# Kernel tuning notes

Hardware: AMD Instinct MI355X
Metric: run time of the kernel (lower is better)

## Reference

```python
import jax, jax.numpy as jnp
import numpy as np

TEMPERATURE = 0.6


def setup_inputs() -> dict:
    key = jax.random.key(0)
    k1, k2, k3 = jax.random.split(key, 3)
    B, IN, OUT, C = 8192, 256, 32, 50
    x = jax.random.uniform(k1, (B, IN), dtype=jnp.float32)
    weight = jax.random.normal(k2, (C, OUT, IN), dtype=jnp.float32) * 0.05
    bias = jax.random.normal(k3, (C, 1, OUT), dtype=jnp.float32) * 0.05
    return {"x": x, "weight": weight, "bias": bias}


def reference(x, weight, bias):
    # gamma[c,i] = L1 norm of weight over out dim: sum_o |W[c,o,i]|
    gamma = jnp.sum(jnp.abs(weight), axis=1)            # [C, IN]
    alpha = jax.nn.softmax(gamma / TEMPERATURE, axis=1)  # [C, IN]
    alpha_norm = alpha / jnp.max(alpha, axis=1, keepdims=True)  # [C, IN]
    # gated input per class: [C, B, IN]
    xg = x[None, :, :] * alpha_norm[:, None, :]
    # per-class GEMM: y[c,b,o] = sum_i xg[c,b,i] * W[c,o,i]
    y = jnp.einsum('cbi,coi->cbo', xg, weight) + bias    # [C, B, OUT]
    return jnp.transpose(y, (1, 0, 2))                   # [B, C, OUT]
```

## Files before the change

kernel.cpp:

```cpp
#include <hip/hip_runtime.h>
#include <hip/hip_bf16.h>

typedef __bf16 bf16x8 __attribute__((ext_vector_type(8)));
typedef float  f32x4  __attribute__((ext_vector_type(4)));

#define B_ROWS 8192
#define IN_DIM 256
#define OUT_DIM 32
#define NCLS 50
#define INV_T (1.0f / 0.6f)

#define CVT_BLOCKS 1024
#define PG_BLOCKS 400
#define ROWTILES 16
#define NCHUNK 8

__device__ __forceinline__ void gload_lds16(const void* g, void* l) {
    __builtin_amdgcn_global_load_lds(
        (const __attribute__((address_space(1))) void*)g,
        (__attribute__((address_space(3))) void*)l, 16, 0, 0);
}

__global__ __launch_bounds__(256) void k1_cvt_partial(const float* __restrict__ x,
                                                      const float* __restrict__ w,
                                                      __bf16* __restrict__ xb,
                                                      float* __restrict__ partial) {
    int bid = blockIdx.x;
    if (bid < CVT_BLOCKS) {
        int i = (bid * 256 + threadIdx.x) * 8;
        float4 v0 = *reinterpret_cast<const float4*>(x + i);
        float4 v1 = *reinterpret_cast<const float4*>(x + i + 4);
        bf16x8 r;
        r[0] = (__bf16)v0.x; r[1] = (__bf16)v0.y; r[2] = (__bf16)v0.z; r[3] = (__bf16)v0.w;
        r[4] = (__bf16)v1.x; r[5] = (__bf16)v1.y; r[6] = (__bf16)v1.z; r[7] = (__bf16)v1.w;
        *reinterpret_cast<bf16x8*>(xb + i) = r;
    } else {
        int p = bid - CVT_BLOCKS;
        int c = p >> 3, q = p & 7;
        int i = threadIdx.x;
        const float* wp = w + ((size_t)(c * OUT_DIM + q * 4)) * IN_DIM + i;
        float g = fabsf(wp[0]) + fabsf(wp[IN_DIM]) + fabsf(wp[2 * IN_DIM]) + fabsf(wp[3 * IN_DIM]);
        partial[(size_t)p * IN_DIM + i] = g;
    }
}

__global__ __launch_bounds__(256) void k2_alpha_scale(const float* __restrict__ partial,
                                                      const float* __restrict__ w,
                                                      __bf16* __restrict__ wb) {
    int blk = blockIdx.x;
    int c = blk >> 2;
    int o0 = (blk & 3) * 8;
    int i = threadIdx.x;
    float g = 0.f;
#pragma unroll
    for (int q = 0; q < 8; ++q)
        g += partial[(size_t)(c * 8 + q) * IN_DIM + i];
    float m = g;
#pragma unroll
    for (int s = 1; s < 64; s <<= 1) m = fmaxf(m, __shfl_xor(m, s));
    __shared__ float wm[4];
    if ((threadIdx.x & 63) == 0) wm[threadIdx.x >> 6] = m;
    __syncthreads();
    m = fmaxf(fmaxf(wm[0], wm[1]), fmaxf(wm[2], wm[3]));
    float an = __expf((g - m) * INV_T);
    const float* wr = w + ((size_t)c * OUT_DIM + o0) * IN_DIM + i;
    __bf16* wo = wb + ((size_t)c * OUT_DIM + o0) * IN_DIM + i;
#pragma unroll
    for (int o = 0; o < 8; ++o)
        wo[o * IN_DIM] = (__bf16)(wr[o * IN_DIM] * an);
}

__global__ __launch_bounds__(256, 2) void gemm(const __bf16* __restrict__ xb,
                                               const __bf16* __restrict__ wb,
                                               const float* __restrict__ bias,
                                               float* __restrict__ out) {
    __shared__ __align__(16) char lds[16384 + 4 * 2 * 8192];

    int bid = blockIdx.x;
    int c = bid >> 4;
    int rt = bid & (ROWTILES - 1);
    int row0 = rt * 512;
    int lane = threadIdx.x & 63;
    int w4 = threadIdx.x >> 6;
    int l15 = lane & 15;
    int g = lane >> 4;

    char* Wlds = lds;
    char* Abuf0 = lds + 16384 + w4 * 16384;
    char* Abuf1 = Abuf0 + 8192;

    const char* arows = (const char*)(xb + (size_t)(row0 + w4 * 128) * IN_DIM);
    int s31 = lane & 31;
    int lr = lane >> 5;
#define STAGE_A(BUF, CHUNK)                                                       \
    _Pragma("unroll") for (int il = 0; il < 8; ++il) {                            \
        int r = (CHUNK) * 16 + 2 * il + lr;                                       \
        gload_lds16(arows + (size_t)r * 512 + ((s31 ^ (r & 15)) * 16),            \
                    (BUF) + il * 1024);                                           \
    }
    STAGE_A(Abuf0, 0)

    const char* wsrc = (const char*)(wb + (size_t)c * OUT_DIM * IN_DIM);
#pragma unroll
    for (int j = 0; j < 4; ++j) {
        int row = j * 8 + w4 * 2 + lr;
        gload_lds16(wsrc + (size_t)row * 512 + ((s31 ^ (row & 15)) * 16),
                    Wlds + j * 4096 + w4 * 1024);
    }

    asm volatile("s_waitcnt vmcnt(0)" ::: "memory");
    __syncthreads();
    __builtin_amdgcn_sched_barrier(0);

    bf16x8 W[16];
#pragma unroll
    for (int kk = 0; kk < 8; ++kk) {
        int slot = (4 * kk + g) ^ l15;
        W[kk]     = *reinterpret_cast<const bf16x8*>(Wlds + (size_t)l15 * 512 + slot * 16);
        W[8 + kk] = *reinterpret_cast<const bf16x8*>(Wlds + (size_t)(16 + l15) * 512 + slot * 16);
    }
#pragma unroll
    for (int kk = 0; kk < 16; ++kk)
        asm volatile("" : "+v"(W[kk]));

    float4 bv0 = *reinterpret_cast<const float4*>(bias + c * OUT_DIM + g * 4);
    float4 bv1 = *reinterpret_cast<const float4*>(bias + c * OUT_DIM + 16 + g * 4);

    float* orow = out + (size_t)(row0 + w4 * 128 + l15) * (NCLS * OUT_DIM) + c * OUT_DIM + g * 4;

#pragma unroll
    for (int k = 0; k < NCHUNK; ++k) {
        char* cur = (k & 1) ? Abuf1 : Abuf0;
        char* nxt = (k & 1) ? Abuf0 : Abuf1;
        if (k + 1 < NCHUNK) {
            STAGE_A(nxt, k + 1)
            asm volatile("s_waitcnt vmcnt(8)" ::: "memory");
        } else {
            asm volatile("s_waitcnt vmcnt(0)" ::: "memory");
        }
        __builtin_amdgcn_sched_barrier(0);

        f32x4 acc0 = {bv0.x, bv0.y, bv0.z, bv0.w};
        f32x4 acc1 = {bv1.x, bv1.y, bv1.z, bv1.w};
#pragma unroll
        for (int kk = 0; kk < 8; ++kk) {
            int slot = (4 * kk + g) ^ l15;
            bf16x8 a = *reinterpret_cast<const bf16x8*>(cur + (size_t)l15 * 512 + slot * 16);
            acc0 = __builtin_amdgcn_mfma_f32_16x16x32_bf16(W[kk],     a, acc0, 0, 0, 0);
            acc1 = __builtin_amdgcn_mfma_f32_16x16x32_bf16(W[8 + kk], a, acc1, 0, 0, 0);
        }
        float* op = orow + (size_t)k * 16 * (NCLS * OUT_DIM);
        *reinterpret_cast<f32x4*>(op) = acc0;
        *reinterpret_cast<f32x4*>(op + 16) = acc1;
    }
#undef STAGE_A
}

extern "C" void kernel_launch(void* const* d_in, const int* in_sizes, int n_in,
                              void* d_out, int out_size, void* d_ws, size_t ws_size,
                              hipStream_t stream) {
    const float* x    = (const float*)d_in[0];
    const float* w    = (const float*)d_in[1];
    const float* bias = (const float*)d_in[2];
    float* out = (float*)d_out;

    __bf16* xb      = (__bf16*)d_ws;
    __bf16* wb      = xb + (size_t)B_ROWS * IN_DIM;
    float*  partial = (float*)(wb + (size_t)NCLS * OUT_DIM * IN_DIM);

    k1_cvt_partial<<<CVT_BLOCKS + PG_BLOCKS, 256, 0, stream>>>(x, w, xb, partial);
    k2_alpha_scale<<<200, 256, 0, stream>>>(partial, w, wb);
    gemm<<<NCLS * ROWTILES, 256, 0, stream>>>(xb, wb, bias, out);
}
```

Baseline: 34.92 us.

## Process two classes per GEMM block to reuse staged x tiles

Each GEMM block now handles two classes, so the x row tile is loaded into LDS once and used for both classes' weights, halving global reads of x. The W staging area is overlaid onto the A double buffers (loaded first, copied to registers, then a barrier), which shrinks LDS per block. The cost is double the weight registers per thread and half as many blocks (400 instead of 800), which lowers parallelism. Store traffic per block doubles, and the output stores for the two classes are contiguous.

After: 30.66 us. 12.2% less time.

```diff
diff --git a/kernel.cpp b/kernel.cpp
--- a/kernel.cpp
+++ b/kernel.cpp
@@ -74,24 +74,24 @@
                                                const __bf16* __restrict__ wb,
                                                const float* __restrict__ bias,
                                                float* __restrict__ out) {
-    __shared__ __align__(16) char lds[16384 + 4 * 2 * 8192];
+    __shared__ __align__(16) char lds[4 * 2 * 8192];
 
     int bid = blockIdx.x;
-    int c = bid >> 4;
+    int cp = bid >> 4;
     int rt = bid & (ROWTILES - 1);
+    int c0 = cp * 2;
     int row0 = rt * 512;
     int lane = threadIdx.x & 63;
     int w4 = threadIdx.x >> 6;
     int l15 = lane & 15;
     int g = lane >> 4;
+    int s31 = lane & 31;
+    int lr = lane >> 5;
 
-    char* Wlds = lds;
-    char* Abuf0 = lds + 16384 + w4 * 16384;
+    char* Abuf0 = lds + w4 * 16384;
     char* Abuf1 = Abuf0 + 8192;
 
     const char* arows = (const char*)(xb + (size_t)(row0 + w4 * 128) * IN_DIM);
-    int s31 = lane & 31;
-    int lr = lane >> 5;
 #define STAGE_A(BUF, CHUNK)                                                       \
     _Pragma("unroll") for (int il = 0; il < 8; ++il) {                            \
         int r = (CHUNK) * 16 + 2 * il + lr;                                       \
@@ -100,33 +100,44 @@
     }
     STAGE_A(Abuf0, 0)
 
-    const char* wsrc = (const char*)(wb + (size_t)c * OUT_DIM * IN_DIM);
+    const char* wsrc = (const char*)(wb + (size_t)c0 * OUT_DIM * IN_DIM);
 #pragma unroll
-    for (int j = 0; j < 4; ++j) {
-        int row = j * 8 + w4 * 2 + lr;
-        gload_lds16(wsrc + (size_t)row * 512 + ((s31 ^ (row & 15)) * 16),
-                    Wlds + j * 4096 + w4 * 1024);
+    for (int j = 0; j < 8; ++j) {
+        int re = j * 8 + w4 * 2;
+        int r = re + lr;
+        gload_lds16(wsrc + (size_t)r * 512 + ((s31 ^ (r & 15)) * 16),
+                    lds + (re >> 4) * 16384 + 8192 + (re & 15) * 512);
     }
 
     asm volatile("s_waitcnt vmcnt(0)" ::: "memory");
     __syncthreads();
     __builtin_amdgcn_sched_barrier(0);
 
-    bf16x8 W[16];
+    bf16x8 W[2][16];
 #pragma unroll
-    for (int kk = 0; kk < 8; ++kk) {
-        int slot = (4 * kk + g) ^ l15;
-        W[kk]     = *reinterpret_cast<const bf16x8*>(Wlds + (size_t)l15 * 512 + slot * 16);
-        W[8 + kk] = *reinterpret_cast<const bf16x8*>(Wlds + (size_t)(16 + l15) * 512 + slot * 16);
-    }
+    for (int ci = 0; ci < 2; ++ci)
 #pragma unroll
-    for (int kk = 0; kk < 16; ++kk)
-        asm volatile("" : "+v"(W[kk]));
+        for (int kk = 0; kk < 8; ++kk) {
+            int slot = (4 * kk + g) ^ l15;
+            W[ci][kk]     = *reinterpret_cast<const bf16x8*>(
+                lds + (2 * ci) * 16384 + 8192 + l15 * 512 + slot * 16);
+            W[ci][8 + kk] = *reinterpret_cast<const bf16x8*>(
+                lds + (2 * ci + 1) * 16384 + 8192 + l15 * 512 + slot * 16);
+        }
+#pragma unroll
+    for (int ci = 0; ci < 2; ++ci)
+#pragma unroll
+        for (int kk = 0; kk < 16; ++kk)
+            asm volatile("" : "+v"(W[ci][kk]));
+    __builtin_amdgcn_sched_barrier(0);
+    __syncthreads();
 
-    float4 bv0 = *reinterpret_cast<const float4*>(bias + c * OUT_DIM + g * 4);
-    float4 bv1 = *reinterpret_cast<const float4*>(bias + c * OUT_DIM + 16 + g * 4);
+    float4 bv00 = *reinterpret_cast<const float4*>(bias + c0 * OUT_DIM + g * 4);
+    float4 bv01 = *reinterpret_cast<const float4*>(bias + c0 * OUT_DIM + 16 + g * 4);
+    float4 bv10 = *reinterpret_cast<const float4*>(bias + (c0 + 1) * OUT_DIM + g * 4);
+    float4 bv11 = *reinterpret_cast<const float4*>(bias + (c0 + 1) * OUT_DIM + 16 + g * 4);
 
-    float* orow = out + (size_t)(row0 + w4 * 128 + l15) * (NCLS * OUT_DIM) + c * OUT_DIM + g * 4;
+    float* orow = out + (size_t)(row0 + w4 * 128 + l15) * (NCLS * OUT_DIM) + c0 * OUT_DIM + g * 4;
 
 #pragma unroll
     for (int k = 0; k < NCHUNK; ++k) {
@@ -134,24 +145,30 @@
         char* nxt = (k & 1) ? Abuf0 : Abuf1;
         if (k + 1 < NCHUNK) {
             STAGE_A(nxt, k + 1)
-            asm volatile("s_waitcnt vmcnt(8)" ::: "memory");
+            asm volatile("s_waitcnt vmcnt(12)" ::: "memory");
         } else {
-            asm volatile("s_waitcnt vmcnt(0)" ::: "memory");
+            asm volatile("s_waitcnt vmcnt(4)" ::: "memory");
         }
         __builtin_amdgcn_sched_barrier(0);
 
-        f32x4 acc0 = {bv0.x, bv0.y, bv0.z, bv0.w};
-        f32x4 acc1 = {bv1.x, bv1.y, bv1.z, bv1.w};
+        f32x4 acc00 = {bv00.x, bv00.y, bv00.z, bv00.w};
+        f32x4 acc01 = {bv01.x, bv01.y, bv01.z, bv01.w};
+        f32x4 acc10 = {bv10.x, bv10.y, bv10.z, bv10.w};
+        f32x4 acc11 = {bv11.x, bv11.y, bv11.z, bv11.w};
 #pragma unroll
         for (int kk = 0; kk < 8; ++kk) {
             int slot = (4 * kk + g) ^ l15;
             bf16x8 a = *reinterpret_cast<const bf16x8*>(cur + (size_t)l15 * 512 + slot * 16);
-            acc0 = __builtin_amdgcn_mfma_f32_16x16x32_bf16(W[kk],     a, acc0, 0, 0, 0);
-            acc1 = __builtin_amdgcn_mfma_f32_16x16x32_bf16(W[8 + kk], a, acc1, 0, 0, 0);
+            acc00 = __builtin_amdgcn_mfma_f32_16x16x32_bf16(W[0][kk],     a, acc00, 0, 0, 0);
+            acc01 = __builtin_amdgcn_mfma_f32_16x16x32_bf16(W[0][8 + kk], a, acc01, 0, 0, 0);
+            acc10 = __builtin_amdgcn_mfma_f32_16x16x32_bf16(W[1][kk],     a, acc10, 0, 0, 0);
+            acc11 = __builtin_amdgcn_mfma_f32_16x16x32_bf16(W[1][8 + kk], a, acc11, 0, 0, 0);
         }
         float* op = orow + (size_t)k * 16 * (NCLS * OUT_DIM);
-        *reinterpret_cast<f32x4*>(op) = acc0;
-        *reinterpret_cast<f32x4*>(op + 16) = acc1;
+        *reinterpret_cast<f32x4*>(op) = acc00;
+        *reinterpret_cast<f32x4*>(op + 16) = acc01;
+        *reinterpret_cast<f32x4*>(op + OUT_DIM) = acc10;
+        *reinterpret_cast<f32x4*>(op + OUT_DIM + 16) = acc11;
     }
 #undef STAGE_A
 }
@@ -170,5 +187,5 @@
 
     k1_cvt_partial<<<CVT_BLOCKS + PG_BLOCKS, 256, 0, stream>>>(x, w, xb, partial);
     k2_alpha_scale<<<200, 256, 0, stream>>>(partial, w, wb);
-    gemm<<<NCLS * ROWTILES, 256, 0, stream>>>(xb, wb, bias, out);
+    gemm<<<25 * ROWTILES, 256, 0, stream>>>(xb, wb, bias, out);
 }
```
